# Kernel tuning notes

Measured on AMD Instinct MI355X. Metric: run time of the kernel, lower is better.

The kernel has to match this reference:

```python
import jax, jax.numpy as jnp
import numpy as np

P, L, D, H, K = 128, 800, 200, 100, 2  # passages, seq_len, input dim, hidden, spans per passage
VOCAB = 30522


def setup_inputs() -> dict:
    key = jax.random.key(0)
    ks = jax.random.split(key, 8)
    S_p = jax.random.normal(ks[0], (P, L, D), dtype=jnp.float32)
    # sorted along last axis so start <= end
    spans = jnp.sort(jax.random.randint(ks[1], (P, K, 2), 0, L), axis=-1)
    passages = jax.random.randint(ks[2], (P, L), 0, VOCAB)
    s = 0.05
    Wb = jax.random.normal(ks[3], (H, D), jnp.float32) * s
    We = jax.random.normal(ks[4], (H, D), jnp.float32) * s
    Wc = jax.random.normal(ks[5], (H, H), jnp.float32) * s
    Wo = jax.random.normal(ks[6], (H, H), jnp.float32) * s
    Wv = jax.random.normal(ks[7], (1, H), jnp.float32) * s
    return {"S_p": S_p, "spans": spans, "passages": passages,
            "Wb": Wb, "We": We, "Wc": Wc, "Wo": Wo, "Wv": Wv}


def reference(S_p, spans, passages, Wb, We, Wc, Wo, Wv):
    M = P * K
    p_idx = jnp.repeat(jnp.arange(P), K)            # [M] passage index per candidate
    starts = spans[:, :, 0].reshape(M)
    ends = spans[:, :, 1].reshape(M)
    t = jnp.arange(L)

    # S_Cs: candidate kept at its original position, zero elsewhere (== F.pad of the slice)
    span_mask = (t[None, :] >= starts[:, None]) & (t[None, :] <= ends[:, None])  # [M, L]
    S_Cs = S_p[p_idx] * span_mask[..., None].astype(S_p.dtype)                   # [M, L, D]

    # encoded candidates: token ids shifted to position 0, right-padded with 0
    gidx = jnp.clip(starts[:, None] + t[None, :], 0, L - 1)                      # [M, L]
    len_mask = t[None, :] <= (ends - starts)[:, None]
    encoded_candidates = jnp.where(len_mask, passages[p_idx[:, None], gidx], 0)  # [M, L]

    # condensed representation from start/end token states
    sb = S_p[p_idx, starts]                          # [M, D]
    se = S_p[p_idx, ends]                            # [M, D]
    r_Cs = jnp.tanh(sb @ Wb.T + se @ We.T)           # [M, H]

    # pairwise scores V_full[i, j] = Wv tanh(Wc r_i + Wo r_j)
    c = r_Cs @ Wc.T                                  # [M, H]
    o = r_Cs @ Wo.T                                  # [M, H]
    V_full = jnp.tanh(c[:, None, :] + o[None, :, :]) @ Wv[0]   # [M, M]

    # leave-one-out gather: V[i] = V_full[i, j != i]
    cols = jnp.arange(M - 1)
    rows = jnp.arange(M)
    idx = cols[None, :] + (cols[None, :] >= rows[:, None]).astype(cols.dtype)    # [M, M-1]
    V = V_full[rows[:, None], idx]                   # [M, M-1]

    # alpha[i] = exp(V[i]) / sum_{j != i} exp(V[j])  (per-column, non-standard normalization)
    E = jnp.exp(V)                                   # [M, M-1]
    denom = E.sum(axis=0, keepdims=True) - E
    alpha = E / denom                                # [M, M-1]

    # tilda_r[i] = sum over rows of (alpha excl row i) @ (r_Cs excl row i)
    s_rows = alpha.sum(axis=0, keepdims=True) - alpha   # [M, M-1]
    R_excl = r_Cs[idx]                                  # [M, M-1, H]
    tilda_r_Cs = jnp.einsum('mb,mbh->mh', s_rows, R_excl)  # [M, H]

    return S_Cs, r_Cs, encoded_candidates, V, tilda_r_Cs
```

## Files before the change

### kernel.cpp

```cpp
#include <hip/hip_runtime.h>
#include <math.h>

#define LP 800
#define DP 200
#define HP 100
#define PP 128
#define KP 2
#define MP 256
#define MM1 255

#define OFF_SCS  0u
#define OFF_R    40960000u
#define OFF_ENC  40985600u
#define OFF_V    41190400u
#define OFF_TIL  41255680u

#define WS_C     0u
#define WS_O     25600u
#define WS_E     51200u
#define WS_ALPHA 116480u
#define WS_COLA  181760u

__global__ void scs_kernel(const float4* __restrict__ Sp4,
                           const int* __restrict__ spans,
                           float4* __restrict__ out4) {
    int m = blockIdx.y;
    int off = blockIdx.x * blockDim.x + threadIdx.x;
    if (off >= 40000) return;
    int p = m >> 1, k = m & 1;
    int start = spans[p * 4 + k * 2];
    int end   = spans[p * 4 + k * 2 + 1];
    int t = off / 50;
    float4 v = make_float4(0.f, 0.f, 0.f, 0.f);
    if (t >= start && t <= end) v = Sp4[p * 40000 + off];
    out4[m * 40000 + off] = v;
}

__global__ void enc_kernel(const int* __restrict__ passages,
                           const int* __restrict__ spans,
                           float* __restrict__ enc) {
    int m = blockIdx.x;
    int p = m >> 1, k = m & 1;
    int start = spans[p * 4 + k * 2];
    int end   = spans[p * 4 + k * 2 + 1];
    int len = end - start;
    for (int t = threadIdx.x; t < LP; t += blockDim.x) {
        int g = start + t; if (g > LP - 1) g = LP - 1;
        int tok = (t <= len) ? passages[p * LP + g] : 0;
        enc[m * LP + t] = (float)tok;
    }
}

__global__ void rco_kernel(const float* __restrict__ Sp,
                           const int* __restrict__ spans,
                           const float* __restrict__ Wb,
                           const float* __restrict__ We,
                           const float* __restrict__ Wc,
                           const float* __restrict__ Wo,
                           float* __restrict__ r_out,
                           float* __restrict__ c_ws,
                           float* __restrict__ o_ws) {
    __shared__ float sb[DP], se[DP], rs[HP];
    int m = blockIdx.x;
    int p = m >> 1, k = m & 1;
    int start = spans[p * 4 + k * 2];
    int end   = spans[p * 4 + k * 2 + 1];
    const float* sbp = Sp + (size_t)(p * LP + start) * DP;
    const float* sep = Sp + (size_t)(p * LP + end) * DP;
    for (int d = threadIdx.x; d < DP; d += blockDim.x) {
        sb[d] = sbp[d];
        se[d] = sep[d];
    }
    __syncthreads();
    int h = threadIdx.x;
    if (h < HP) {
        const float* wb = Wb + h * DP;
        const float* we = We + h * DP;
        float acc = 0.f;
        for (int d = 0; d < DP; ++d) acc += sb[d] * wb[d] + se[d] * we[d];
        float r = tanhf(acc);
        rs[h] = r;
        r_out[m * HP + h] = r;
    }
    __syncthreads();
    if (h < HP) {
        const float* wc = Wc + h * HP;
        const float* wo = Wo + h * HP;
        float accc = 0.f, acco = 0.f;
        for (int hp = 0; hp < HP; ++hp) {
            float r = rs[hp];
            accc += r * wc[hp];
            acco += r * wo[hp];
        }
        c_ws[m * HP + h] = accc;
        o_ws[m * HP + h] = acco;
    }
}

__global__ void v_kernel(const float* __restrict__ c_ws,
                         const float* __restrict__ o_ws,
                         const float* __restrict__ Wv,
                         float* __restrict__ V_out,
                         float* __restrict__ E_ws) {
    __shared__ float cs[HP], wv[HP];
    int i = blockIdx.x;
    if (threadIdx.x < HP) {
        cs[threadIdx.x] = c_ws[i * HP + threadIdx.x];
        wv[threadIdx.x] = Wv[threadIdx.x];
    }
    __syncthreads();
    int jp = threadIdx.x;
    if (jp < MM1) {
        int j = jp + (jp >= i ? 1 : 0);
        const float* oj = o_ws + j * HP;
        float acc = 0.f;
        for (int h = 0; h < HP; ++h) acc += tanhf(cs[h] + oj[h]) * wv[h];
        V_out[i * MM1 + jp] = acc;
        E_ws[i * MM1 + jp] = expf(acc);
    }
}

__global__ void alpha_kernel(const float* __restrict__ E_ws,
                             float* __restrict__ alpha_ws,
                             float* __restrict__ colA_ws) {
    int jp = threadIdx.x;
    if (jp >= MM1) return;
    float colE = 0.f;
    for (int i = 0; i < MP; ++i) colE += E_ws[i * MM1 + jp];
    float colA = 0.f;
    for (int i = 0; i < MP; ++i) {
        float e = E_ws[i * MM1 + jp];
        float a = e / (colE - e);
        alpha_ws[i * MM1 + jp] = a;
        colA += a;
    }
    colA_ws[jp] = colA;
}

__global__ void tilda_kernel(const float* __restrict__ alpha_ws,
                             const float* __restrict__ colA_ws,
                             const float* __restrict__ r_out,
                             float* __restrict__ til_out) {
    __shared__ float s[MM1];
    int i = blockIdx.x;
    for (int jp = threadIdx.x; jp < MM1; jp += blockDim.x)
        s[jp] = colA_ws[jp] - alpha_ws[i * MM1 + jp];
    __syncthreads();
    int h = threadIdx.x;
    if (h < HP) {
        float acc = 0.f;
        for (int jp = 0; jp < MM1; ++jp) {
            int j = jp + (jp >= i ? 1 : 0);
            acc += s[jp] * r_out[j * HP + h];
        }
        til_out[i * HP + h] = acc;
    }
}

extern "C" void kernel_launch(void* const* d_in, const int* in_sizes, int n_in,
                              void* d_out, int out_size, void* d_ws, size_t ws_size,
                              hipStream_t stream) {
    const float* S_p      = (const float*)d_in[0];
    const int*   spans    = (const int*)d_in[1];
    const int*   passages = (const int*)d_in[2];
    const float* Wb       = (const float*)d_in[3];
    const float* We       = (const float*)d_in[4];
    const float* Wc       = (const float*)d_in[5];
    const float* Wo       = (const float*)d_in[6];
    const float* Wv       = (const float*)d_in[7];

    float* out = (float*)d_out;
    float* ws  = (float*)d_ws;

    float* out_scs = out + OFF_SCS;
    float* out_r   = out + OFF_R;
    float* out_enc = out + OFF_ENC;
    float* out_v   = out + OFF_V;
    float* out_til = out + OFF_TIL;

    float* ws_c     = ws + WS_C;
    float* ws_o     = ws + WS_O;
    float* ws_e     = ws + WS_E;
    float* ws_alpha = ws + WS_ALPHA;
    float* ws_colA  = ws + WS_COLA;

    dim3 gridA((40000 + 255) / 256, MP);
    scs_kernel<<<gridA, 256, 0, stream>>>((const float4*)S_p, spans, (float4*)out_scs);

    enc_kernel<<<MP, 256, 0, stream>>>(passages, spans, out_enc);

    rco_kernel<<<MP, 128, 0, stream>>>(S_p, spans, Wb, We, Wc, Wo, out_r, ws_c, ws_o);

    v_kernel<<<MP, 256, 0, stream>>>(ws_c, ws_o, Wv, out_v, ws_e);

    alpha_kernel<<<1, 256, 0, stream>>>(ws_e, ws_alpha, ws_colA);

    tilda_kernel<<<MP, 128, 0, stream>>>(ws_alpha, ws_colA, out_r, out_til);
}
```

Measured before the change: 325.8 us.

## Parallelize column normalization across blocks and fuse small kernels with fast math

Replaces the single-block alpha kernel with one block per column using wave shuffle reductions. It also precomputes the per-row exclusion weights so the tilda kernel reads them directly. The encoded-candidates kernel is merged into the r/c/o kernel. Loads are vectorized, tanh and exp are replaced with fast exp-based approximations, and S_Cs stores become nontemporal. This trades some floating-point accuracy for removing a serial bottleneck and extra launches.

After: 277.4 us. -14.9%, faster.

```diff
diff --git a/kernel.cpp b/kernel.cpp
--- a/kernel.cpp
+++ b/kernel.cpp
@@ -4,10 +4,10 @@
 #define LP 800
 #define DP 200
 #define HP 100
-#define PP 128
-#define KP 2
 #define MP 256
 #define MM1 255
+
+typedef float fx4 __attribute__((ext_vector_type(4)));
 
 #define OFF_SCS  0u
 #define OFF_R    40960000u
@@ -18,12 +18,16 @@
 #define WS_C     0u
 #define WS_O     25600u
 #define WS_E     51200u
-#define WS_ALPHA 116480u
-#define WS_COLA  181760u
-
-__global__ void scs_kernel(const float4* __restrict__ Sp4,
-                           const int* __restrict__ spans,
-                           float4* __restrict__ out4) {
+#define WS_S     116480u
+
+__device__ __forceinline__ float tanh_fast(float x) {
+    float e = __expf(2.0f * x);
+    return 1.0f - 2.0f / (e + 1.0f);
+}
+
+__global__ __launch_bounds__(256) void scs_kernel(const fx4* __restrict__ Sp4,
+                                                  const int* __restrict__ spans,
+                                                  fx4* __restrict__ out4) {
     int m = blockIdx.y;
     int off = blockIdx.x * blockDim.x + threadIdx.x;
     if (off >= 40000) return;
@@ -31,128 +35,148 @@
     int start = spans[p * 4 + k * 2];
     int end   = spans[p * 4 + k * 2 + 1];
     int t = off / 50;
-    float4 v = make_float4(0.f, 0.f, 0.f, 0.f);
+    fx4 v = (fx4)(0.f);
     if (t >= start && t <= end) v = Sp4[p * 40000 + off];
-    out4[m * 40000 + off] = v;
-}
-
-__global__ void enc_kernel(const int* __restrict__ passages,
-                           const int* __restrict__ spans,
-                           float* __restrict__ enc) {
+    __builtin_nontemporal_store(v, &out4[m * 40000 + off]);
+}
+
+__global__ __launch_bounds__(256) void encrco_kernel(const float* __restrict__ Sp,
+                                                     const int* __restrict__ spans,
+                                                     const int* __restrict__ passages,
+                                                     const float* __restrict__ Wb,
+                                                     const float* __restrict__ We,
+                                                     const float* __restrict__ Wc,
+                                                     const float* __restrict__ Wo,
+                                                     float* __restrict__ enc,
+                                                     float* __restrict__ r_out,
+                                                     float* __restrict__ c_ws,
+                                                     float* __restrict__ o_ws) {
+    __shared__ float4 sb4[50], se4[50], rs4[25];
     int m = blockIdx.x;
     int p = m >> 1, k = m & 1;
     int start = spans[p * 4 + k * 2];
     int end   = spans[p * 4 + k * 2 + 1];
+    int tid = threadIdx.x;
+
     int len = end - start;
-    for (int t = threadIdx.x; t < LP; t += blockDim.x) {
+    for (int t = tid; t < LP; t += 256) {
         int g = start + t; if (g > LP - 1) g = LP - 1;
-        int tok = (t <= len) ? passages[p * LP + g] : 0;
-        enc[m * LP + t] = (float)tok;
-    }
-}
-
-__global__ void rco_kernel(const float* __restrict__ Sp,
-                           const int* __restrict__ spans,
-                           const float* __restrict__ Wb,
-                           const float* __restrict__ We,
-                           const float* __restrict__ Wc,
-                           const float* __restrict__ Wo,
-                           float* __restrict__ r_out,
-                           float* __restrict__ c_ws,
-                           float* __restrict__ o_ws) {
-    __shared__ float sb[DP], se[DP], rs[HP];
-    int m = blockIdx.x;
-    int p = m >> 1, k = m & 1;
-    int start = spans[p * 4 + k * 2];
-    int end   = spans[p * 4 + k * 2 + 1];
-    const float* sbp = Sp + (size_t)(p * LP + start) * DP;
-    const float* sep = Sp + (size_t)(p * LP + end) * DP;
-    for (int d = threadIdx.x; d < DP; d += blockDim.x) {
-        sb[d] = sbp[d];
-        se[d] = sep[d];
-    }
-    __syncthreads();
-    int h = threadIdx.x;
+        enc[m * LP + t] = (t <= len) ? (float)passages[p * LP + g] : 0.f;
+    }
+
+    const float4* sbp = (const float4*)(Sp + (size_t)(p * LP + start) * DP);
+    const float4* sep = (const float4*)(Sp + (size_t)(p * LP + end) * DP);
+    if (tid < 50)       sb4[tid]      = sbp[tid];
+    else if (tid < 100) se4[tid - 50] = sep[tid - 50];
+    __syncthreads();
+
+    int h = tid;
     if (h < HP) {
-        const float* wb = Wb + h * DP;
-        const float* we = We + h * DP;
+        const float4* wb = (const float4*)(Wb + h * DP);
+        const float4* we = (const float4*)(We + h * DP);
         float acc = 0.f;
-        for (int d = 0; d < DP; ++d) acc += sb[d] * wb[d] + se[d] * we[d];
-        float r = tanhf(acc);
-        rs[h] = r;
+        #pragma unroll
+        for (int d = 0; d < 50; ++d) {
+            float4 a = sb4[d], b = wb[d];
+            acc += a.x * b.x + a.y * b.y + a.z * b.z + a.w * b.w;
+            float4 a2 = se4[d], b2 = we[d];
+            acc += a2.x * b2.x + a2.y * b2.y + a2.z * b2.z + a2.w * b2.w;
+        }
+        float r = tanh_fast(acc);
+        ((float*)rs4)[h] = r;
         r_out[m * HP + h] = r;
     }
     __syncthreads();
     if (h < HP) {
-        const float* wc = Wc + h * HP;
-        const float* wo = Wo + h * HP;
+        const float4* wc = (const float4*)(Wc + h * HP);
+        const float4* wo = (const float4*)(Wo + h * HP);
         float accc = 0.f, acco = 0.f;
-        for (int hp = 0; hp < HP; ++hp) {
-            float r = rs[hp];
-            accc += r * wc[hp];
-            acco += r * wo[hp];
+        #pragma unroll
+        for (int q = 0; q < 25; ++q) {
+            float4 r = rs4[q], cc = wc[q], oo = wo[q];
+            accc += r.x * cc.x + r.y * cc.y + r.z * cc.z + r.w * cc.w;
+            acco += r.x * oo.x + r.y * oo.y + r.z * oo.z + r.w * oo.w;
         }
         c_ws[m * HP + h] = accc;
         o_ws[m * HP + h] = acco;
     }
 }
 
-__global__ void v_kernel(const float* __restrict__ c_ws,
-                         const float* __restrict__ o_ws,
-                         const float* __restrict__ Wv,
-                         float* __restrict__ V_out,
-                         float* __restrict__ E_ws) {
-    __shared__ float cs[HP], wv[HP];
+__global__ __launch_bounds__(256) void v_kernel(const float* __restrict__ c_ws,
+                                                const float* __restrict__ o_ws,
+                                                const float* __restrict__ Wv,
+                                                float* __restrict__ V_out,
+                                                float* __restrict__ E_ws) {
+    __shared__ float4 cs4[25], wv4[25];
     int i = blockIdx.x;
-    if (threadIdx.x < HP) {
-        cs[threadIdx.x] = c_ws[i * HP + threadIdx.x];
-        wv[threadIdx.x] = Wv[threadIdx.x];
-    }
-    __syncthreads();
-    int jp = threadIdx.x;
+    int tid = threadIdx.x;
+    if (tid < 25) {
+        cs4[tid] = ((const float4*)(c_ws + i * HP))[tid];
+        wv4[tid] = ((const float4*)Wv)[tid];
+    }
+    __syncthreads();
+    int jp = tid;
     if (jp < MM1) {
         int j = jp + (jp >= i ? 1 : 0);
-        const float* oj = o_ws + j * HP;
+        const float4* oj = (const float4*)(o_ws + j * HP);
         float acc = 0.f;
-        for (int h = 0; h < HP; ++h) acc += tanhf(cs[h] + oj[h]) * wv[h];
+        #pragma unroll
+        for (int q = 0; q < 25; ++q) {
+            float4 o4 = oj[q], c4 = cs4[q], w4 = wv4[q];
+            acc += tanh_fast(c4.x + o4.x) * w4.x;
+            acc += tanh_fast(c4.y + o4.y) * w4.y;
+            acc += tanh_fast(c4.z + o4.z) * w4.z;
+            acc += tanh_fast(c4.w + o4.w) * w4.w;
+        }
         V_out[i * MM1 + jp] = acc;
-        E_ws[i * MM1 + jp] = expf(acc);
-    }
-}
-
-__global__ void alpha_kernel(const float* __restrict__ E_ws,
-                             float* __restrict__ alpha_ws,
-                             float* __restrict__ colA_ws) {
-    int jp = threadIdx.x;
-    if (jp >= MM1) return;
-    float colE = 0.f;
-    for (int i = 0; i < MP; ++i) colE += E_ws[i * MM1 + jp];
-    float colA = 0.f;
-    for (int i = 0; i < MP; ++i) {
-        float e = E_ws[i * MM1 + jp];
-        float a = e / (colE - e);
-        alpha_ws[i * MM1 + jp] = a;
-        colA += a;
-    }
-    colA_ws[jp] = colA;
-}
-
-__global__ void tilda_kernel(const float* __restrict__ alpha_ws,
-                             const float* __restrict__ colA_ws,
-                             const float* __restrict__ r_out,
-                             float* __restrict__ til_out) {
-    __shared__ float s[MM1];
+        E_ws[i * MM1 + jp] = __expf(acc);
+    }
+}
+
+__global__ __launch_bounds__(256) void alpha_kernel(const float* __restrict__ E_ws,
+                                                    float* __restrict__ s_ws) {
+    __shared__ float partial[4];
+    int jp = blockIdx.x;
+    int i = threadIdx.x;
+    float e = E_ws[i * MM1 + jp];
+
+    float v = e;
+    v += __shfl_down(v, 32); v += __shfl_down(v, 16); v += __shfl_down(v, 8);
+    v += __shfl_down(v, 4);  v += __shfl_down(v, 2);  v += __shfl_down(v, 1);
+    if ((i & 63) == 0) partial[i >> 6] = v;
+    __syncthreads();
+    float colE = partial[0] + partial[1] + partial[2] + partial[3];
+
+    float a = e / (colE - e);
+
+    __syncthreads();
+    float v2 = a;
+    v2 += __shfl_down(v2, 32); v2 += __shfl_down(v2, 16); v2 += __shfl_down(v2, 8);
+    v2 += __shfl_down(v2, 4);  v2 += __shfl_down(v2, 2);  v2 += __shfl_down(v2, 1);
+    if ((i & 63) == 0) partial[i >> 6] = v2;
+    __syncthreads();
+    float colA = partial[0] + partial[1] + partial[2] + partial[3];
+
+    s_ws[i * MM1 + jp] = colA - a;
+}
+
+__global__ __launch_bounds__(128) void tilda_kernel(const float* __restrict__ s_ws,
+                                                    const float* __restrict__ r_out,
+                                                    float* __restrict__ til_out) {
+    __shared__ float s[MM1 + 1];
     int i = blockIdx.x;
-    for (int jp = threadIdx.x; jp < MM1; jp += blockDim.x)
-        s[jp] = colA_ws[jp] - alpha_ws[i * MM1 + jp];
+    for (int jp = threadIdx.x; jp < MM1; jp += 128)
+        s[jp] = s_ws[i * MM1 + jp];
     __syncthreads();
     int h = threadIdx.x;
     if (h < HP) {
         float acc = 0.f;
-        for (int jp = 0; jp < MM1; ++jp) {
-            int j = jp + (jp >= i ? 1 : 0);
-            acc += s[jp] * r_out[j * HP + h];
-        }
+        #pragma unroll 4
+        for (int jp = 0; jp < i; ++jp)
+            acc += s[jp] * r_out[jp * HP + h];
+        #pragma unroll 4
+        for (int jp = i; jp < MM1; ++jp)
+            acc += s[jp] * r_out[(jp + 1) * HP + h];
         til_out[i * HP + h] = acc;
     }
 }
@@ -178,22 +202,17 @@
     float* out_v   = out + OFF_V;
     float* out_til = out + OFF_TIL;
 
-    float* ws_c     = ws + WS_C;
-    float* ws_o     = ws + WS_O;
-    float* ws_e     = ws + WS_E;
-    float* ws_alpha = ws + WS_ALPHA;
-    float* ws_colA  = ws + WS_COLA;
+    float* ws_c = ws + WS_C;
+    float* ws_o = ws + WS_O;
+    float* ws_e = ws + WS_E;
+    float* ws_s = ws + WS_S;
+
+    encrco_kernel<<<MP, 256, 0, stream>>>(S_p, spans, passages, Wb, We, Wc, Wo,
+                                          out_enc, out_r, ws_c, ws_o);
+    v_kernel<<<MP, 256, 0, stream>>>(ws_c, ws_o, Wv, out_v, ws_e);
+    alpha_kernel<<<MM1, 256, 0, stream>>>(ws_e, ws_s);
+    tilda_kernel<<<MP, 128, 0, stream>>>(ws_s, out_r, out_til);
 
     dim3 gridA((40000 + 255) / 256, MP);
-    scs_kernel<<<gridA, 256, 0, stream>>>((const float4*)S_p, spans, (float4*)out_scs);
-
-    enc_kernel<<<MP, 256, 0, stream>>>(passages, spans, out_enc);
-
-    rco_kernel<<<MP, 128, 0, stream>>>(S_p, spans, Wb, We, Wc, Wo, out_r, ws_c, ws_o);
-
-    v_kernel<<<MP, 256, 0, stream>>>(ws_c, ws_o, Wv, out_v, ws_e);
-
-    alpha_kernel<<<1, 256, 0, stream>>>(ws_e, ws_alpha, ws_colA);
-
-    tilda_kernel<<<MP, 128, 0, stream>>>(ws_alpha, ws_colA, out_r, out_til);
-}
+    scs_kernel<<<gridA, 256, 0, stream>>>((const fx4*)S_p, spans, (fx4*)out_scs);
+}
```
